# Performance work log

Hardware: AMD Instinct MI355X
Metric: run time of the kernel (lower is better)

The kernel has to match this reference:

```python
import jax, jax.numpy as jnp
import numpy as np

N_E = 4096
E_DIM = 64
BETA = 0.25


def setup_inputs() -> dict:
    key = jax.random.key(0)
    k1, k2 = jax.random.split(key)
    z = jax.random.normal(k1, (16, E_DIM, 32, 32), dtype=jnp.float32)
    embedding = jax.random.normal(k2, (N_E, E_DIM), dtype=jnp.float32)
    return {"z": z, "embedding": embedding}


def reference(z, embedding):
    # b c h w -> b h w c
    zc = jnp.transpose(z, (0, 2, 3, 1))  # [B,H,W,C]
    B, H, W, C = zc.shape
    zf = zc.reshape(-1, C)  # [N, C]

    # Squared Euclidean distances (argmin is identical to cdist p=2 argmin)
    # d2[n,e] = |z|^2 - 2 z.e + |e|^2
    d2 = (
        jnp.sum(zf * zf, axis=1, keepdims=True)
        - 2.0 * (zf @ embedding.T)
        + jnp.sum(embedding * embedding, axis=1)[None, :]
    )  # [N, n_e]
    idx = jnp.argmin(d2, axis=1)  # [N]

    z_q = embedding[idx].reshape(B, H, W, C)

    # dist_p == 2 losses
    loss_d1 = jnp.mean((jax.lax.stop_gradient(z_q) - zc) ** 2)
    loss_d2 = jnp.mean((z_q - jax.lax.stop_gradient(zc)) ** 2)
    loss = BETA * loss_d1 + loss_d2

    # Straight-through estimator
    z_q = zc + jax.lax.stop_gradient(z_q - zc)

    indices = idx.reshape(B, H, W)
    z_q = jnp.transpose(z_q, (0, 3, 1, 2))  # b h w c -> b c h w
    return z_q, loss, indices
```

## Files before the change

kernel.cpp:

```cpp
#include <hip/hip_runtime.h>

typedef float f32x4 __attribute__((ext_vector_type(4)));
typedef short bf16x8 __attribute__((ext_vector_type(8)));

#define HW_ 1024
#define NE_ 4096
#define CHW_ 65536
#define ZQ_SIZE 1048576
#define LOSS_OFF ZQ_SIZE
#define IDX_OFF (ZQ_SIZE + 1)
#define LOSS_SCALE (1.25f / 1048576.f)
#define EPS_GAP 0.1f

union FragU { unsigned u[4]; bf16x8 v; };

__device__ __forceinline__ unsigned umin_(unsigned a, unsigned b) { return a < b ? a : b; }
__device__ __forceinline__ unsigned umax_(unsigned a, unsigned b) { return a > b ? a : b; }

__device__ __forceinline__ void split8(const float* v, FragU& hi, FragU& lo) {
#pragma unroll
    for (int p = 0; p < 4; p++) {
        float a = v[2 * p], b = v[2 * p + 1];
        unsigned ua = __float_as_uint(a), ub = __float_as_uint(b);
        hi.u[p] = (ua >> 16) | (ub & 0xFFFF0000u);
        float la = a - __uint_as_float(ua & 0xFFFF0000u);
        float lb = b - __uint_as_float(ub & 0xFFFF0000u);
        lo.u[p] = (__float_as_uint(la) >> 16) | (__float_as_uint(lb) & 0xFFFF0000u);
    }
}

__device__ __forceinline__ void gload_lds16(const void* g, void* l) {
    __builtin_amdgcn_global_load_lds(
        (const __attribute__((address_space(1))) unsigned*)g,
        (__attribute__((address_space(3))) unsigned*)l, 16, 0, 0);
}

__global__ __launch_bounds__(256) void vq_pre(
        const float* __restrict__ z, const float* __restrict__ emb,
        float* __restrict__ h_e, float* __restrict__ h_z,
        char* __restrict__ zfrag, char* __restrict__ efrag,
        float* __restrict__ out) {
    const int bid = blockIdx.x, tid = threadIdx.x;
    if (bid < 512) {
        __shared__ float red[2][2][16];
        int u = bid * 256 + tid;
        int l = u & 63, s = (u >> 6) & 1, t = u >> 7;
        int n = t * 16 + (l & 15);
        int b = n >> 10, hw = n & 1023;
        int c0 = s * 32 + (l >> 4) * 8;
        const float* zp = z + (size_t)b * CHW_ + hw;
        float v[8];
        float ss = 0.f;
#pragma unroll
        for (int j = 0; j < 8; j++) {
            v[j] = zp[(c0 + j) * HW_];
            ss = fmaf(v[j], v[j], ss);
        }
        FragU hi, lo;
        split8(v, hi, lo);
        char* base = zfrag + (size_t)t * 4096 + l * 16;
        *(FragU*)(base + s * 1024) = hi;
        *(FragU*)(base + (2 + s) * 1024) = lo;
        ss += __shfl_xor(ss, 16);
        ss += __shfl_xor(ss, 32);
        if ((l >> 4) == 0) red[tid >> 7][s][l & 15] = ss;
        __syncthreads();
        if (tid < 32) {
            int tt = tid >> 4, r = tid & 15;
            h_z[(bid * 2 + tt) * 16 + r] = 0.5f * (red[tt][0][r] + red[tt][1][r]);
        }
    } else if (bid < 640) {
        int u = (bid - 512) * 256 + tid;
        int l = u & 63, s = (u >> 6) & 1, t = u >> 7;
        int er = t * 16 + (l & 15);
        int c0 = s * 32 + (l >> 4) * 8;
        const float* ep = emb + (size_t)er * 64 + c0;
        float4 ea = *(const float4*)(ep);
        float4 eb = *(const float4*)(ep + 4);
        float v[8];
        v[0] = -ea.x; v[1] = -ea.y; v[2] = -ea.z; v[3] = -ea.w;
        v[4] = -eb.x; v[5] = -eb.y; v[6] = -eb.z; v[7] = -eb.w;
        FragU hi, lo;
        split8(v, hi, lo);
        char* base = efrag + (size_t)t * 4096 + l * 16;
        *(FragU*)(base + s * 1024) = hi;
        *(FragU*)(base + (2 + s) * 1024) = lo;
    } else {
        int t = (bid - 640) * 256 + tid;
        const float4* er = (const float4*)(emb + (size_t)t * 64);
        float s = 0.f;
#pragma unroll
        for (int k = 0; k < 16; k++) {
            float4 e4 = er[k];
            s = fmaf(e4.x, e4.x, s); s = fmaf(e4.y, e4.y, s);
            s = fmaf(e4.z, e4.z, s); s = fmaf(e4.w, e4.w, s);
        }
        h_e[t] = 0.5f * s;
        if (t == 0) out[LOSS_OFF] = 0.f;
    }
}

__global__ __launch_bounds__(512) void vq_mfma(
        const char* __restrict__ zfrag, const char* __restrict__ efrag,
        const float* __restrict__ h_e, const float* __restrict__ h_z,
        unsigned* __restrict__ k1q, unsigned* __restrict__ k2q) {
    __shared__ char buf[2][32768];
    __shared__ __attribute__((aligned(16))) float sh_he[512];

    const int tid = threadIdx.x;
    const int lane = tid & 63;
    const int w = tid >> 6;
    const int lrow = lane & 15;
    const int lgrp = lane >> 4;
    const int es = blockIdx.x & 7;
    const int rb = blockIdx.x >> 3;
    const int e0t = es * 32;
    const int rt0 = rb * 32 + w * 4;

    sh_he[tid] = h_e[es * 512 + tid];

    {
        const char* src = efrag + (size_t)(e0t + w) * 4096 + lane * 16;
        char* dst = buf[0] + w * 4096;
#pragma unroll
        for (int i = 0; i < 4; i++) gload_lds16(src + i * 1024, dst + i * 1024);
    }

    bf16x8 zh[4][2], zl[4][2];
    float hz[4];
#pragma unroll
    for (int r = 0; r < 4; r++) {
        const char* zb = zfrag + (size_t)(rt0 + r) * 4096 + lane * 16;
        zh[r][0] = *(const bf16x8*)(zb);
        zh[r][1] = *(const bf16x8*)(zb + 1024);
        zl[r][0] = *(const bf16x8*)(zb + 2048);
        zl[r][1] = *(const bf16x8*)(zb + 3072);
        hz[r] = h_z[(rt0 + r) * 16 + lrow];
    }

    unsigned s1k[4] = {~0u, ~0u, ~0u, ~0u};
    unsigned s2k[4] = {~0u, ~0u, ~0u, ~0u};

    __syncthreads();
    for (int c = 0; c < 4; c++) {
        if (c < 3) {
            const char* src = efrag + (size_t)(e0t + (c + 1) * 8 + w) * 4096
                              + lane * 16;
            char* dst = buf[(c + 1) & 1] + w * 4096;
#pragma unroll
            for (int i = 0; i < 4; i++) gload_lds16(src + i * 1024, dst + i * 1024);
        }

        const char* cb = buf[c & 1] + lane * 16;
#pragma unroll
        for (int j = 0; j < 8; j++) {
            const char* tb = cb + j * 4096;
            bf16x8 ah0 = *(const bf16x8*)(tb);
            bf16x8 ah1 = *(const bf16x8*)(tb + 1024);
            bf16x8 al0 = *(const bf16x8*)(tb + 2048);
            bf16x8 al1 = *(const bf16x8*)(tb + 3072);
            const int etl = c * 8 + j;
            const f32x4 he = *(const f32x4*)&sh_he[etl * 16 + lgrp * 4];

            f32x4 a0 = he + hz[0], a1 = he + hz[1];
            f32x4 a2 = he + hz[2], a3 = he + hz[3];

            a0 = __builtin_amdgcn_mfma_f32_16x16x32_bf16(ah0, zh[0][0], a0, 0, 0, 0);
            a1 = __builtin_amdgcn_mfma_f32_16x16x32_bf16(ah0, zh[1][0], a1, 0, 0, 0);
            a2 = __builtin_amdgcn_mfma_f32_16x16x32_bf16(ah0, zh[2][0], a2, 0, 0, 0);
            a3 = __builtin_amdgcn_mfma_f32_16x16x32_bf16(ah0, zh[3][0], a3, 0, 0, 0);
            a0 = __builtin_amdgcn_mfma_f32_16x16x32_bf16(ah1, zh[0][1], a0, 0, 0, 0);
            a1 = __builtin_amdgcn_mfma_f32_16x16x32_bf16(ah1, zh[1][1], a1, 0, 0, 0);
            a2 = __builtin_amdgcn_mfma_f32_16x16x32_bf16(ah1, zh[2][1], a2, 0, 0, 0);
            a3 = __builtin_amdgcn_mfma_f32_16x16x32_bf16(ah1, zh[3][1], a3, 0, 0, 0);
            a0 = __builtin_amdgcn_mfma_f32_16x16x32_bf16(al0, zh[0][0], a0, 0, 0, 0);
            a1 = __builtin_amdgcn_mfma_f32_16x16x32_bf16(al0, zh[1][0], a1, 0, 0, 0);
            a2 = __builtin_amdgcn_mfma_f32_16x16x32_bf16(al0, zh[2][0], a2, 0, 0, 0);
            a3 = __builtin_amdgcn_mfma_f32_16x16x32_bf16(al0, zh[3][0], a3, 0, 0, 0);
            a0 = __builtin_amdgcn_mfma_f32_16x16x32_bf16(al1, zh[0][1], a0, 0, 0, 0);
            a1 = __builtin_amdgcn_mfma_f32_16x16x32_bf16(al1, zh[1][1], a1, 0, 0, 0);
            a2 = __builtin_amdgcn_mfma_f32_16x16x32_bf16(al1, zh[2][1], a2, 0, 0, 0);
            a3 = __builtin_amdgcn_mfma_f32_16x16x32_bf16(al1, zh[3][1], a3, 0, 0, 0);
            a0 = __builtin_amdgcn_mfma_f32_16x16x32_bf16(ah0, zl[0][0], a0, 0, 0, 0);
            a1 = __builtin_amdgcn_mfma_f32_16x16x32_bf16(ah0, zl[1][0], a1, 0, 0, 0);
            a2 = __builtin_amdgcn_mfma_f32_16x16x32_bf16(ah0, zl[2][0], a2, 0, 0, 0);
            a3 = __builtin_amdgcn_mfma_f32_16x16x32_bf16(ah0, zl[3][0], a3, 0, 0, 0);
            a0 = __builtin_amdgcn_mfma_f32_16x16x32_bf16(ah1, zl[0][1], a0, 0, 0, 0);
            a1 = __builtin_amdgcn_mfma_f32_16x16x32_bf16(ah1, zl[1][1], a1, 0, 0, 0);
            a2 = __builtin_amdgcn_mfma_f32_16x16x32_bf16(ah1, zl[2][1], a2, 0, 0, 0);
            a3 = __builtin_amdgcn_mfma_f32_16x16x32_bf16(ah1, zl[3][1], a3, 0, 0, 0);

            const unsigned eb12 = (unsigned)(es * 512 + etl * 16 + lgrp * 4);
#pragma unroll
            for (int rr = 0; rr < 4; rr++) {
                unsigned key0 = (__float_as_uint(a0[rr]) & 0xFFFFF000u) | (eb12 + rr);
                s2k[0] = umin_(s2k[0], umax_(s1k[0], key0));
                s1k[0] = umin_(s1k[0], key0);
                unsigned key1 = (__float_as_uint(a1[rr]) & 0xFFFFF000u) | (eb12 + rr);
                s2k[1] = umin_(s2k[1], umax_(s1k[1], key1));
                s1k[1] = umin_(s1k[1], key1);
                unsigned key2 = (__float_as_uint(a2[rr]) & 0xFFFFF000u) | (eb12 + rr);
                s2k[2] = umin_(s2k[2], umax_(s1k[2], key2));
                s1k[2] = umin_(s1k[2], key2);
                unsigned key3 = (__float_as_uint(a3[rr]) & 0xFFFFF000u) | (eb12 + rr);
                s2k[3] = umin_(s2k[3], umax_(s1k[3], key3));
                s1k[3] = umin_(s1k[3], key3);
            }
        }
        __syncthreads();
    }

#pragma unroll
    for (int off = 16; off <= 32; off += 16) {
#pragma unroll
        for (int r = 0; r < 4; r++) {
            unsigned o1 = (unsigned)__shfl_xor((int)s1k[r], off);
            unsigned o2 = (unsigned)__shfl_xor((int)s2k[r], off);
            s2k[r] = umin_(umin_(s2k[r], o2), umax_(s1k[r], o1));
            s1k[r] = umin_(s1k[r], o1);
        }
    }

    if (lane < 16) {
        const int base = es * 16384;
#pragma unroll
        for (int r = 0; r < 4; r++) {
            k1q[base + (rt0 + r) * 16 + lane] = s1k[r];
            k2q[base + (rt0 + r) * 16 + lane] = s2k[r];
        }
    }
}

__global__ __launch_bounds__(256) void vq_final(
        const float* __restrict__ z, const float* __restrict__ emb,
        const unsigned* __restrict__ k1q, const unsigned* __restrict__ k2q,
        float* __restrict__ out) {
    int t = blockIdx.x * 256 + threadIdx.x;
    int n = t & 16383;
    int q = t >> 14;

    unsigned m = 0xFFFFFFFFu, s = 0xFFFFFFFFu;
#pragma unroll
    for (int i = 0; i < 8; i++) {
        unsigned a = k1q[i * 16384 + n];
        unsigned b = k2q[i * 16384 + n];
        unsigned hi = umax_(m, a);
        m = umin_(m, a);
        s = umin_(umin_(s, b), hi);
    }

    int idx = (int)(m & 0xFFFu);
    float s1 = __uint_as_float(m & 0xFFFFF000u);
    float s2 = __uint_as_float(s & 0xFFFFF000u);

    int b = n >> 10, hw = n & 1023;
    const float* zp = z + (size_t)b * CHW_ + hw;
    const int cq = q * 16;

    if (s2 - s1 < EPS_GAP) {
        int i2 = (int)(s & 0xFFFu);
        const float* ea = emb + (size_t)idx * 64;
        const float* eb = emb + (size_t)i2 * 64;
        double da = 0.0, db = 0.0;
#pragma unroll 8
        for (int c = 0; c < 64; c++) {
            double zv = (double)zp[c * HW_];
            double xa = (double)ea[c] - zv;
            double xb = (double)eb[c] - zv;
            da = fma(xa, xa, da);
            db = fma(xb, xb, db);
        }
        if (db < da || (db == da && i2 < idx)) idx = i2;
    }

    const float* er = emb + (size_t)idx * 64 + cq;
    float* zq = out + (size_t)b * CHW_ + hw;
    float lsum = 0.f;
#pragma unroll
    for (int j = 0; j < 16; j++) {
        float e = er[j];
        float d = e - zp[(cq + j) * HW_];
        zq[(cq + j) * HW_] = e;
        lsum = fmaf(d, d, lsum);
    }
    if (q == 0) out[IDX_OFF + n] = (float)idx;

#pragma unroll
    for (int off = 32; off; off >>= 1) lsum += __shfl_down(lsum, off);
    if ((threadIdx.x & 63) == 0) atomicAdd(&out[LOSS_OFF], lsum * LOSS_SCALE);
}

extern "C" void kernel_launch(void* const* d_in, const int* in_sizes, int n_in,
                              void* d_out, int out_size, void* d_ws, size_t ws_size,
                              hipStream_t stream) {
    const float* z   = (const float*)d_in[0];
    const float* emb = (const float*)d_in[1];
    float* out = (float*)d_out;
    char* ws = (char*)d_ws;

    char* efrag   = ws;
    char* zfrag   = ws + 1048576;
    float* h_e    = (float*)(ws + 5242880);
    float* h_z    = (float*)(ws + 5259264);
    unsigned* k1q = (unsigned*)(ws + 5324800);
    unsigned* k2q = (unsigned*)(ws + 5849088);

    vq_pre  <<<656, 256, 0, stream>>>(z, emb, h_e, h_z, zfrag, efrag, out);
    vq_mfma <<<256, 512, 0, stream>>>(zfrag, efrag, h_e, h_z, k1q, k2q);
    vq_final<<<256, 256, 0, stream>>>(z, emb, k1q, k2q, out);
}
```

Measured before the change: 56.32 us.

## Fuse z fragment prep into MFMA kernel and fold final pass via last-block counter

Removes the separate z-fragment/h_z staging by having the MFMA kernel load z directly and split it into bf16 hi/lo fragments in registers, along with the row norm. The final argmin-merge, z_q write and loss pass now runs inside the MFMA kernel: a per-row-block atomic counter picks the last of the 8 embedding-slice blocks to do it. This cuts a launch and a global round trip of z fragments. In exchange the last block does the epilogue serially with fewer threads per row (64 channels per thread), and the gather of z is strided.

```diff
diff --git a/kernel.cpp b/kernel.cpp
--- a/kernel.cpp
+++ b/kernel.cpp
@@ -35,42 +35,13 @@
         (__attribute__((address_space(3))) unsigned*)l, 16, 0, 0);
 }
 
-__global__ __launch_bounds__(256) void vq_pre(
-        const float* __restrict__ z, const float* __restrict__ emb,
-        float* __restrict__ h_e, float* __restrict__ h_z,
-        char* __restrict__ zfrag, char* __restrict__ efrag,
+__global__ __launch_bounds__(256) void vq_eprep(
+        const float* __restrict__ emb, char* __restrict__ efrag,
+        float* __restrict__ h_e, unsigned* __restrict__ cnt,
         float* __restrict__ out) {
     const int bid = blockIdx.x, tid = threadIdx.x;
-    if (bid < 512) {
-        __shared__ float red[2][2][16];
+    if (bid < 128) {
         int u = bid * 256 + tid;
-        int l = u & 63, s = (u >> 6) & 1, t = u >> 7;
-        int n = t * 16 + (l & 15);
-        int b = n >> 10, hw = n & 1023;
-        int c0 = s * 32 + (l >> 4) * 8;
-        const float* zp = z + (size_t)b * CHW_ + hw;
-        float v[8];
-        float ss = 0.f;
-#pragma unroll
-        for (int j = 0; j < 8; j++) {
-            v[j] = zp[(c0 + j) * HW_];
-            ss = fmaf(v[j], v[j], ss);
-        }
-        FragU hi, lo;
-        split8(v, hi, lo);
-        char* base = zfrag + (size_t)t * 4096 + l * 16;
-        *(FragU*)(base + s * 1024) = hi;
-        *(FragU*)(base + (2 + s) * 1024) = lo;
-        ss += __shfl_xor(ss, 16);
-        ss += __shfl_xor(ss, 32);
-        if ((l >> 4) == 0) red[tid >> 7][s][l & 15] = ss;
-        __syncthreads();
-        if (tid < 32) {
-            int tt = tid >> 4, r = tid & 15;
-            h_z[(bid * 2 + tt) * 16 + r] = 0.5f * (red[tt][0][r] + red[tt][1][r]);
-        }
-    } else if (bid < 640) {
-        int u = (bid - 512) * 256 + tid;
         int l = u & 63, s = (u >> 6) & 1, t = u >> 7;
         int er = t * 16 + (l & 15);
         int c0 = s * 32 + (l >> 4) * 8;
@@ -85,8 +56,8 @@
         char* base = efrag + (size_t)t * 4096 + l * 16;
         *(FragU*)(base + s * 1024) = hi;
         *(FragU*)(base + (2 + s) * 1024) = lo;
-    } else {
-        int t = (bid - 640) * 256 + tid;
+    } else if (bid < 144) {
+        int t = (bid - 128) * 256 + tid;
         const float4* er = (const float4*)(emb + (size_t)t * 64);
         float s = 0.f;
 #pragma unroll
@@ -96,16 +67,20 @@
             s = fmaf(e4.z, e4.z, s); s = fmaf(e4.w, e4.w, s);
         }
         h_e[t] = 0.5f * s;
-        if (t == 0) out[LOSS_OFF] = 0.f;
+    } else {
+        if (tid < 32) cnt[tid] = 0;
+        if (tid == 32) out[LOSS_OFF] = 0.f;
     }
 }
 
 __global__ __launch_bounds__(512) void vq_mfma(
-        const char* __restrict__ zfrag, const char* __restrict__ efrag,
-        const float* __restrict__ h_e, const float* __restrict__ h_z,
-        unsigned* __restrict__ k1q, unsigned* __restrict__ k2q) {
+        const float* __restrict__ z, const float* __restrict__ emb,
+        const char* __restrict__ efrag, const float* __restrict__ h_e,
+        unsigned* __restrict__ k1q, unsigned* __restrict__ k2q,
+        unsigned* __restrict__ cnt, float* __restrict__ out) {
     __shared__ char buf[2][32768];
     __shared__ __attribute__((aligned(16))) float sh_he[512];
+    __shared__ int s_last;
 
     const int tid = threadIdx.x;
     const int lane = tid & 63;
@@ -116,6 +91,7 @@
     const int rb = blockIdx.x >> 3;
     const int e0t = es * 32;
     const int rt0 = rb * 32 + w * 4;
+    const int b = rb >> 1;
 
     sh_he[tid] = h_e[es * 512 + tid];
 
@@ -130,12 +106,26 @@
     float hz[4];
 #pragma unroll
     for (int r = 0; r < 4; r++) {
-        const char* zb = zfrag + (size_t)(rt0 + r) * 4096 + lane * 16;
-        zh[r][0] = *(const bf16x8*)(zb);
-        zh[r][1] = *(const bf16x8*)(zb + 1024);
-        zl[r][0] = *(const bf16x8*)(zb + 2048);
-        zl[r][1] = *(const bf16x8*)(zb + 3072);
-        hz[r] = h_z[(rt0 + r) * 16 + lrow];
+        float ss = 0.f;
+#pragma unroll
+        for (int s = 0; s < 2; s++) {
+            const int hw = ((rt0 + r) * 16 + lrow) & 1023;
+            const int c0 = s * 32 + lgrp * 8;
+            const float* zp = z + (size_t)b * CHW_ + hw;
+            float v[8];
+#pragma unroll
+            for (int j = 0; j < 8; j++) {
+                v[j] = zp[(c0 + j) * HW_];
+                ss = fmaf(v[j], v[j], ss);
+            }
+            FragU hi, lo;
+            split8(v, hi, lo);
+            zh[r][s] = hi.v;
+            zl[r][s] = lo.v;
+        }
+        ss += __shfl_xor(ss, 16);
+        ss += __shfl_xor(ss, 32);
+        hz[r] = 0.5f * ss;
     }
 
     unsigned s1k[4] = {~0u, ~0u, ~0u, ~0u};
@@ -229,65 +219,63 @@
             k2q[base + (rt0 + r) * 16 + lane] = s2k[r];
         }
     }
-}
-
-__global__ __launch_bounds__(256) void vq_final(
-        const float* __restrict__ z, const float* __restrict__ emb,
-        const unsigned* __restrict__ k1q, const unsigned* __restrict__ k2q,
-        float* __restrict__ out) {
-    int t = blockIdx.x * 256 + threadIdx.x;
-    int n = t & 16383;
-    int q = t >> 14;
-
-    unsigned m = 0xFFFFFFFFu, s = 0xFFFFFFFFu;
-#pragma unroll
-    for (int i = 0; i < 8; i++) {
-        unsigned a = k1q[i * 16384 + n];
-        unsigned b = k2q[i * 16384 + n];
-        unsigned hi = umax_(m, a);
-        m = umin_(m, a);
-        s = umin_(umin_(s, b), hi);
-    }
-
-    int idx = (int)(m & 0xFFFu);
-    float s1 = __uint_as_float(m & 0xFFFFF000u);
-    float s2 = __uint_as_float(s & 0xFFFFF000u);
-
-    int b = n >> 10, hw = n & 1023;
-    const float* zp = z + (size_t)b * CHW_ + hw;
-    const int cq = q * 16;
-
-    if (s2 - s1 < EPS_GAP) {
-        int i2 = (int)(s & 0xFFFu);
-        const float* ea = emb + (size_t)idx * 64;
-        const float* eb = emb + (size_t)i2 * 64;
-        double da = 0.0, db = 0.0;
+
+    __threadfence();
+    __syncthreads();
+    if (tid == 0) s_last = (atomicAdd(&cnt[rb], 1u) == 7u);
+    __syncthreads();
+    if (!s_last) return;
+    __threadfence();
+
+    {
+        const int n = rb * 512 + tid;
+        unsigned m = ~0u, s = ~0u;
+#pragma unroll
+        for (int i = 0; i < 8; i++) {
+            unsigned a = k1q[i * 16384 + n];
+            unsigned bb = k2q[i * 16384 + n];
+            unsigned hi = umax_(m, a);
+            m = umin_(m, a);
+            s = umin_(umin_(s, bb), hi);
+        }
+        int idx = (int)(m & 0xFFFu);
+        float sc1 = __uint_as_float(m & 0xFFFFF000u);
+        float sc2 = __uint_as_float(s & 0xFFFFF000u);
+
+        const int hw = n & 1023;
+        const float* zp = z + (size_t)b * CHW_ + hw;
+
+        if (sc2 - sc1 < EPS_GAP) {
+            int i2 = (int)(s & 0xFFFu);
+            const float* ea = emb + (size_t)idx * 64;
+            const float* eb2 = emb + (size_t)i2 * 64;
+            double da = 0.0, db = 0.0;
 #pragma unroll 8
+            for (int c = 0; c < 64; c++) {
+                double zv = (double)zp[c * HW_];
+                double xa = (double)ea[c] - zv;
+                double xb = (double)eb2[c] - zv;
+                da = fma(xa, xa, da);
+                db = fma(xb, xb, db);
+            }
+            if (db < da || (db == da && i2 < idx)) idx = i2;
+        }
+        out[IDX_OFF + n] = (float)idx;
+
+        const float* er = emb + (size_t)idx * 64;
+        float* zq = out + (size_t)b * CHW_ + hw;
+        float lsum = 0.f;
+#pragma unroll
         for (int c = 0; c < 64; c++) {
-            double zv = (double)zp[c * HW_];
-            double xa = (double)ea[c] - zv;
-            double xb = (double)eb[c] - zv;
-            da = fma(xa, xa, da);
-            db = fma(xb, xb, db);
-        }
-        if (db < da || (db == da && i2 < idx)) idx = i2;
-    }
-
-    const float* er = emb + (size_t)idx * 64 + cq;
-    float* zq = out + (size_t)b * CHW_ + hw;
-    float lsum = 0.f;
-#pragma unroll
-    for (int j = 0; j < 16; j++) {
-        float e = er[j];
-        float d = e - zp[(cq + j) * HW_];
-        zq[(cq + j) * HW_] = e;
-        lsum = fmaf(d, d, lsum);
-    }
-    if (q == 0) out[IDX_OFF + n] = (float)idx;
-
-#pragma unroll
-    for (int off = 32; off; off >>= 1) lsum += __shfl_down(lsum, off);
-    if ((threadIdx.x & 63) == 0) atomicAdd(&out[LOSS_OFF], lsum * LOSS_SCALE);
+            float e = er[c];
+            float d = e - zp[c * HW_];
+            zq[c * HW_] = e;
+            lsum = fmaf(d, d, lsum);
+        }
+#pragma unroll
+        for (int off = 32; off; off >>= 1) lsum += __shfl_down(lsum, off);
+        if (lane == 0) atomicAdd(&out[LOSS_OFF], lsum * LOSS_SCALE);
+    }
 }
 
 extern "C" void kernel_launch(void* const* d_in, const int* in_sizes, int n_in,
@@ -299,13 +287,11 @@
     char* ws = (char*)d_ws;
 
     char* efrag   = ws;
-    char* zfrag   = ws + 1048576;
-    float* h_e    = (float*)(ws + 5242880);
-    float* h_z    = (float*)(ws + 5259264);
-    unsigned* k1q = (unsigned*)(ws + 5324800);
-    unsigned* k2q = (unsigned*)(ws + 5849088);
-
-    vq_pre  <<<656, 256, 0, stream>>>(z, emb, h_e, h_z, zfrag, efrag, out);
-    vq_mfma <<<256, 512, 0, stream>>>(zfrag, efrag, h_e, h_z, k1q, k2q);
-    vq_final<<<256, 256, 0, stream>>>(z, emb, k1q, k2q, out);
-}
+    float* h_e    = (float*)(ws + 1048576);
+    unsigned* k1q = (unsigned*)(ws + 1065024);
+    unsigned* k2q = (unsigned*)(ws + 1589312);
+    unsigned* cnt = (unsigned*)(ws + 2113600);
+
+    vq_eprep<<<145, 256, 0, stream>>>(emb, efrag, h_e, cnt, out);
+    vq_mfma <<<256, 512, 0, stream>>>(z, emb, efrag, h_e, k1q, k2q, cnt, out);
+}
```

Result: slower. 104.5 us (+85.6%).
